# Performance work log

Measured on AMD Instinct MI355X. Metric: run time of the kernel, lower is better.

Reference implementation:

```python
import jax, jax.numpy as jnp
import numpy as np

N_WIRES = 4
N_LAYERS = 2
BSZ = 4096


def setup_inputs() -> dict:
    key = jax.random.key(0)
    k1, k2, k3 = jax.random.split(key, 3)
    return {
        "x": jax.random.normal(k1, (BSZ, 784), dtype=jnp.float32),
        "params": jax.random.normal(k2, (N_LAYERS, N_WIRES), dtype=jnp.float32),
        "W": jax.random.normal(k3, (10, 784), dtype=jnp.float32) * 0.03,
        "b": jnp.zeros((10,), dtype=jnp.float32),
    }


def _rz(state, theta, w):
    # RZ(theta) = diag(exp(-i theta/2), exp(+i theta/2)) on wire w (axis w+1)
    ph = jnp.exp(jnp.array([-0.5j, 0.5j], dtype=jnp.complex64) * theta)
    shape = [1, 1, 1, 1, 1]
    shape[w + 1] = 2
    return state * ph.reshape(shape)


def _cx(state, cw, tw):
    # CNOT with control cw, target tw (tw > cw): flip target axis where control=1
    s0 = jnp.take(state, 0, axis=cw + 1)
    s1 = jnp.take(state, 1, axis=cw + 1)
    s1 = jnp.flip(s1, axis=tw)  # after removing control axis, target axis index = tw
    return jnp.stack([s0, s1], axis=cw + 1)


def quantum_block(patch, params):
    # patch: [N, 4] angles; returns [N, 4] PauliZ expectations
    half = 0.5 * patch
    # RY(theta)|0> = [cos(theta/2), sin(theta/2)]
    amps = jnp.stack([jnp.cos(half), jnp.sin(half)], axis=-1).astype(jnp.complex64)  # [N,4,2]
    state = jnp.einsum('na,nb,nc,nd->nabcd', amps[:, 0], amps[:, 1], amps[:, 2], amps[:, 3])
    for i in range(N_LAYERS):
        for w in range(N_WIRES):
            state = _rz(state, params[i, w], w)
        for w in range(N_WIRES - 1):
            state = _cx(state, w, w + 1)
    probs = state.real ** 2 + state.imag ** 2  # [N,2,2,2,2]
    z = jnp.array([1.0, -1.0], dtype=jnp.float32)
    exps = []
    for w in range(N_WIRES):
        shape = [1, 1, 1, 1, 1]
        shape[w + 1] = 2
        exps.append(jnp.sum(probs * z.reshape(shape), axis=(1, 2, 3, 4)))
    return jnp.stack(exps, axis=-1)  # [N,4]


def reference(x, params, W, b):
    B = x.shape[0]
    # extract 2x2 patches in row-major (r, c) order, each flattened row-major
    img = x.reshape(B, 14, 2, 14, 2).transpose(0, 1, 3, 2, 4).reshape(B * 196, 4)
    feats = quantum_block(img, params).reshape(B, 196 * 4)  # [B, 784]
    logits = feats @ W.T + b
    return jax.nn.log_softmax(logits, axis=-1)
```

## Files before the change

### kernel.cpp

```cpp
#include <hip/hip_runtime.h>
#include <math.h>


#define BSZ 4096

__global__ __launch_bounds__(256) void quanv_fused_kernel(
    const float* __restrict__ x,
    const float* __restrict__ W,
    const float* __restrict__ bias,
    float* __restrict__ out)
{
    __shared__ float sW[10 * 784];

    {
        const float4* Wv = (const float4*)W;
        float4* sWv = (float4*)sW;
        #pragma unroll
        for (int i = 0; i < 8; ++i) {
            int idx = threadIdx.x + i * 256;
            if (idx < 1960) sWv[idx] = Wv[idx];
        }
    }
    __syncthreads();

    const int wave = threadIdx.x >> 6;
    const int lane = threadIdx.x & 63;
    const int row  = blockIdx.x * 4 + wave;

    const float* __restrict__ xr = x + row * 784;

    float acc[10];
    #pragma unroll
    for (int o = 0; o < 10; ++o) acc[o] = 0.f;

    #pragma unroll
    for (int t = 0; t < 4; ++t) {
        const int k = t * 64 + lane;
        if (k < 196) {
            const int r = k / 14;
            const int c = k - r * 14;
            const int base = r * 56 + c * 2;
            const float2 a01 = *(const float2*)(xr + base);
            const float2 a23 = *(const float2*)(xr + base + 28);
            const float f0 = __cosf(a01.x);
            const float f1 = __cosf(a01.y);
            const float f2 = f0 * __cosf(a23.x);
            const float f3 = f1 * __cosf(a23.y);
            const float* wk = sW + k * 4;
            #pragma unroll
            for (int o = 0; o < 10; ++o) {
                const float4 w4 = *(const float4*)(wk + o * 784);
                acc[o] = fmaf(f0, w4.x, acc[o]);
                acc[o] = fmaf(f1, w4.y, acc[o]);
                acc[o] = fmaf(f2, w4.z, acc[o]);
                acc[o] = fmaf(f3, w4.w, acc[o]);
            }
        }
    }

    #pragma unroll
    for (int o = 0; o < 10; ++o) {
        float v = acc[o];
        #pragma unroll
        for (int s = 32; s >= 1; s >>= 1) v += __shfl_xor(v, s, 64);
        acc[o] = v + bias[o];
    }

    float m = acc[0];
    #pragma unroll
    for (int o = 1; o < 10; ++o) m = fmaxf(m, acc[o]);
    float sum = 0.f;
    #pragma unroll
    for (int o = 0; o < 10; ++o) sum += __expf(acc[o] - m);
    const float lse = __logf(sum);

    if (lane < 10) out[row * 10 + lane] = acc[lane] - m - lse;
}

extern "C" void kernel_launch(void* const* d_in, const int* in_sizes, int n_in,
                              void* d_out, int out_size, void* d_ws, size_t ws_size,
                              hipStream_t stream) {
    const float* x    = (const float*)d_in[0];
    const float* W    = (const float*)d_in[2];
    const float* bias = (const float*)d_in[3];
    float* out = (float*)d_out;

    dim3 grid(BSZ / 4);
    dim3 block(256);
    quanv_fused_kernel<<<grid, block, 0, stream>>>(x, W, bias, out);
}
```

Baseline: 12.12 us.

## Process two rows per wave and reduce with DPP row operations

```diff
diff --git a/kernel.cpp b/kernel.cpp
--- a/kernel.cpp
+++ b/kernel.cpp
@@ -4,7 +4,11 @@
 
 #define BSZ 4096
 
-__global__ __launch_bounds__(256) void quanv_fused_kernel(
+#define DPP_ADD(v, ctrl, rmask)                                              \
+    v += __int_as_float(__builtin_amdgcn_update_dpp(                         \
+        0, __float_as_int(v), (ctrl), (rmask), 0xf, true))
+
+__global__ __launch_bounds__(256) void quanv_fused_v2(
     const float* __restrict__ x,
     const float* __restrict__ W,
     const float* __restrict__ bias,
@@ -23,9 +27,12 @@
     }
     __syncthreads();
 
-    const int wave = threadIdx.x >> 6;
-    const int lane = threadIdx.x & 63;
-    const int row  = blockIdx.x * 4 + wave;
+    const int tid  = threadIdx.x;
+    const int wave = tid >> 6;
+    const int lane = tid & 63;
+    const int h    = lane >> 5;
+    const int kl   = lane & 31;
+    const int row  = blockIdx.x * 8 + wave * 2 + h;
 
     const float* __restrict__ xr = x + row * 784;
 
@@ -34,9 +41,9 @@
     for (int o = 0; o < 10; ++o) acc[o] = 0.f;
 
     #pragma unroll
-    for (int t = 0; t < 4; ++t) {
-        const int k = t * 64 + lane;
-        if (k < 196) {
+    for (int t = 0; t < 7; ++t) {
+        const int k = t * 32 + kl;
+        if (t < 6 || kl < 4) {
             const int r = k / 14;
             const int c = k - r * 14;
             const int base = r * 56 + c * 2;
@@ -61,20 +68,30 @@
     #pragma unroll
     for (int o = 0; o < 10; ++o) {
         float v = acc[o];
-        #pragma unroll
-        for (int s = 32; s >= 1; s >>= 1) v += __shfl_xor(v, s, 64);
-        acc[o] = v + bias[o];
+        DPP_ADD(v, 0x111, 0xf);
+        DPP_ADD(v, 0x112, 0xf);
+        DPP_ADD(v, 0x114, 0xf);
+        DPP_ADD(v, 0x118, 0xf);
+        DPP_ADD(v, 0x142, 0xa);
+        acc[o] = v;
     }
 
-    float m = acc[0];
-    #pragma unroll
-    for (int o = 1; o < 10; ++o) m = fmaxf(m, acc[o]);
-    float sum = 0.f;
-    #pragma unroll
-    for (int o = 0; o < 10; ++o) sum += __expf(acc[o] - m);
-    const float lse = __logf(sum);
-
-    if (lane < 10) out[row * 10 + lane] = acc[lane] - m - lse;
+    if (kl == 31) {
+        float lg[10];
+        float m = -1e30f;
+        #pragma unroll
+        for (int o = 0; o < 10; ++o) {
+            lg[o] = acc[o] + bias[o];
+            m = fmaxf(m, lg[o]);
+        }
+        float s = 0.f;
+        #pragma unroll
+        for (int o = 0; o < 10; ++o) s += __expf(lg[o] - m);
+        const float lse = __logf(s) + m;
+        float* orow = out + row * 10;
+        #pragma unroll
+        for (int o = 0; o < 10; ++o) orow[o] = lg[o] - lse;
+    }
 }
 
 extern "C" void kernel_launch(void* const* d_in, const int* in_sizes, int n_in,
@@ -85,7 +102,7 @@
     const float* bias = (const float*)d_in[3];
     float* out = (float*)d_out;
 
-    dim3 grid(BSZ / 4);
+    dim3 grid(BSZ / 8);
     dim3 block(256);
-    quanv_fused_kernel<<<grid, block, 0, stream>>>(x, W, bias, out);
+    quanv_fused_v2<<<grid, block, 0, stream>>>(x, W, bias, out);
 }
```

After: 9.977 us. 1.21x faster.
